# Kernel optimization log

Measured on AMD Instinct MI355X. Metric: run time of the kernel, lower is better.

The kernel has to match this reference:

```python
import jax, jax.numpy as jnp
import numpy as np

GROUPS = 32
N_HEADS = 16
EPS = 1e-5


def setup_inputs() -> dict:
    key = jax.random.key(0)
    ks = jax.random.split(key, 5)
    b, c, t = 4, 1024, 1024
    return {
        "x": jax.random.normal(ks[0], (b, c, t), dtype=jnp.float32),
        "gn_weight": jnp.ones((c,), dtype=jnp.float32),
        "gn_bias": jnp.zeros((c,), dtype=jnp.float32),
        "qkv_w": jax.random.normal(ks[1], (3 * c, c), dtype=jnp.float32) * (c ** -0.5),
        "qkv_b": jax.random.normal(ks[2], (3 * c,), dtype=jnp.float32) * 0.02,
        "proj_w": jax.random.normal(ks[3], (c, c), dtype=jnp.float32) * (c ** -0.5),
        "proj_b": jax.random.normal(ks[4], (c,), dtype=jnp.float32) * 0.02,
    }


def _group_norm(x, weight, bias):
    # x: [b, c, t]; GroupNorm32 computes stats in float32 (already fp32 here)
    b, c, t = x.shape
    xg = x.reshape(b, GROUPS, c // GROUPS, t)
    mean = xg.mean(axis=(2, 3), keepdims=True)
    var = xg.var(axis=(2, 3), keepdims=True)
    xn = ((xg - mean) * jax.lax.rsqrt(var + EPS)).reshape(b, c, t)
    return xn * weight[None, :, None] + bias[None, :, None]


def reference(x, gn_weight, gn_bias, qkv_w, qkv_b, proj_w, proj_b):
    b, c, t = x.shape
    xn = _group_norm(x, gn_weight, gn_bias)
    # 1x1 Conv1d == channel matmul: [3c, c] x [b, c, t] -> [b, 3c, t]
    qkv = jnp.einsum('oc,bct->bot', qkv_w, xn) + qkv_b[None, :, None]
    ch = c // N_HEADS
    # legacy per-head interleaved layout: reshape to [b*H, 3*ch, t], split
    qkv = qkv.reshape(b * N_HEADS, 3 * ch, t)
    q, k, v = qkv[:, :ch], qkv[:, ch:2 * ch], qkv[:, 2 * ch:]
    scale = ch ** -0.25  # 1/sqrt(sqrt(ch)), applied to both q and k
    weight = jnp.einsum('bct,bcs->bts', q * scale, k * scale)  # [b*H, t, t]
    weight = jax.nn.softmax(weight.astype(jnp.float32), axis=-1).astype(weight.dtype)
    a = jnp.einsum('bts,bcs->bct', weight, v).reshape(b, c, t)
    h = jnp.einsum('oc,bct->bot', proj_w, a) + proj_b[None, :, None]
    return x + h
```

## Files before the change

### kernel.cpp

```cpp
#include <hip/hip_runtime.h>
#include <hip/hip_bf16.h>

typedef __bf16 bf16;
typedef __bf16 bf16x2 __attribute__((ext_vector_type(2)));
typedef __bf16 bf16x4 __attribute__((ext_vector_type(4)));
typedef __bf16 bf16x8 __attribute__((ext_vector_type(8)));
typedef float  f32x4  __attribute__((ext_vector_type(4)));

static __device__ __forceinline__ f32x4 mfma16(bf16x8 a, bf16x8 b, f32x4 c) {
  return __builtin_amdgcn_mfma_f32_16x16x32_bf16(a, b, c, 0, 0, 0);
}

static __device__ __forceinline__ void gload_lds16(const bf16* g, bf16* l) {
  __builtin_amdgcn_global_load_lds(
      (const __attribute__((address_space(1))) void*)g,
      (__attribute__((address_space(3))) void*)l, 16, 0, 0);
}

#define VMCNT0() asm volatile("s_waitcnt vmcnt(0)" ::: "memory")
#define BARRIER()                                        \
  do {                                                   \
    __builtin_amdgcn_sched_barrier(0);                   \
    asm volatile("" ::: "memory");                       \
    __builtin_amdgcn_s_barrier();                        \
    asm volatile("" ::: "memory");                       \
    __builtin_amdgcn_sched_barrier(0);                   \
  } while (0)

__global__ __launch_bounds__(256) void cvt2_kernel(const float* __restrict__ wa,
                                                   bf16* __restrict__ oa,
                                                   const float* __restrict__ wb,
                                                   bf16* __restrict__ ob) {
  int i = blockIdx.x * 256 + threadIdx.x;
  const int na4 = 3072 * 1024 / 4;
  const float* src; bf16* dst;
  if (i < na4) { src = wa; dst = oa; }
  else         { src = wb; dst = ob; i -= na4; }
  float4 v = ((const float4*)src)[i];
  bf16x4 o = { (bf16)v.x, (bf16)v.y, (bf16)v.z, (bf16)v.w };
  *(bf16x4*)(dst + 4ll * i) = o;
}

__global__ __launch_bounds__(512) void gn_kernel(const float* __restrict__ x,
                                                 const float* __restrict__ w,
                                                 const float* __restrict__ bias,
                                                 bf16* __restrict__ xnT) {
  int id = blockIdx.x;
  int b = id >> 7, g = (id >> 2) & 31, qtr = id & 3;
  const float* xb = x + ((size_t)b * 1024 + g * 32) * 1024;
  int tid = threadIdx.x;
  float s = 0.f, sq = 0.f;
  const float4* x4 = (const float4*)xb;
  for (int i = tid; i < 8192; i += 512) {
    float4 v = x4[i];
    s  += v.x + v.y + v.z + v.w;
    sq += v.x * v.x + v.y * v.y + v.z * v.z + v.w * v.w;
  }
#pragma unroll
  for (int off = 32; off; off >>= 1) { s += __shfl_down(s, off); sq += __shfl_down(sq, off); }
  __shared__ float red[16];
  int wv = tid >> 6;
  if ((tid & 63) == 0) { red[wv] = s; red[8 + wv] = sq; }
  __syncthreads();
  s = 0.f; sq = 0.f;
#pragma unroll
  for (int i = 0; i < 8; ++i) { s += red[i]; sq += red[8 + i]; }
  float mean = s * (1.f / 32768.f);
  float var  = sq * (1.f / 32768.f) - mean * mean;
  float rstd = rsqrtf(var + 1e-5f);

  __shared__ bf16 tile[64][36];
  int c = tid >> 4, q = tid & 15;
  int r = tid >> 3, q2 = tid & 7;
  float wc = w[g * 32 + c] * rstd;
  float fb = bias[g * 32 + c] - mean * wc;
  for (int t0 = qtr * 256; t0 < qtr * 256 + 256; t0 += 64) {
    float4 v = *(const float4*)(xb + (size_t)c * 1024 + t0 + q * 4);
    tile[q * 4 + 0][c] = (bf16)(v.x * wc + fb);
    tile[q * 4 + 1][c] = (bf16)(v.y * wc + fb);
    tile[q * 4 + 2][c] = (bf16)(v.z * wc + fb);
    tile[q * 4 + 3][c] = (bf16)(v.w * wc + fb);
    __syncthreads();
    *(bf16x4*)&xnT[((size_t)b * 1024 + t0 + r) * 1024 + g * 32 + q2 * 4] =
        *(bf16x4*)&tile[r][q2 * 4];
    __syncthreads();
  }
}

__global__ __launch_bounds__(512, 1) void qkv_kernel(
    const bf16* __restrict__ A, const bf16* __restrict__ Bw,
    const float* __restrict__ bias,
    bf16* __restrict__ qkT, bf16* __restrict__ vC) {
  extern __shared__ __align__(16) bf16 smem[];

  int tid = threadIdx.x, wid = tid >> 6, lane = tid & 63;
  int l15 = lane & 15, l4 = lane >> 4;
  int wr = wid >> 2, wc = wid & 3;
  int rsw = (l15 & 7) << 4;

  int sid = (blockIdx.x & 7) * 32 + (blockIdx.x >> 3);
  int bx = sid & 15, by = (sid >> 4) & 3, z = sid >> 6;
  int m0 = by * 256, n0 = bx * 192;
  const bf16* Ab = A + (size_t)z * 1024 * 1024 + (size_t)m0 * 1024;
  const bf16* Bb = Bw + (size_t)n0 * 1024;

  int srow = tid >> 3;
  int csw  = (tid & 7) ^ (srow & 7);
  auto stageA = [&](int d, int h, int kt) {
    bf16* dst = smem + d * 16384 + h * 8192;
    const bf16* src = Ab + (size_t)(h * 128) * 1024 + kt * 64 + csw * 8;
#pragma unroll
    for (int L = 0; L < 2; ++L)
      gload_lds16(src + (size_t)(L * 64 + srow) * 1024, dst + (L * 512 + wid * 64) * 8);
  };
  auto stageB = [&](int d, int kt) {
    bf16* dst = smem + 32768 + d * 12288;
    const bf16* src = Bb + kt * 64 + csw * 8;
#pragma unroll
    for (int L = 0; L < 3; ++L)
      gload_lds16(src + (size_t)(L * 64 + srow) * 1024, dst + (L * 512 + wid * 64) * 8);
  };

  f32x4 acc[8][3] = {};

  stageA(0, 0, 0); stageA(0, 1, 0); stageB(0, 0);
  VMCNT0();
  BARRIER();

  for (int t = 0; t < 16; ++t) {
    int d = t & 1;
    const char* Ab8 = (const char*)smem + d * 32768 + wr * 16384;
    const char* Bb8 = (const char*)smem + 65536 + d * 24576;

    bf16x8 bfr[3][2], af[4][2];
#pragma unroll
    for (int ni = 0; ni < 3; ++ni) {
      int rb = (wc * 48 + ni * 16 + l15) * 128;
#pragma unroll
      for (int kk = 0; kk < 2; ++kk)
        bfr[ni][kk] = *(const bf16x8*)(Bb8 + rb + ((kk * 64 + l4 * 16) ^ rsw));
    }
#pragma unroll
    for (int mi = 0; mi < 4; ++mi) {
      int rb = (mi * 16 + l15) * 128;
#pragma unroll
      for (int kk = 0; kk < 2; ++kk)
        af[mi][kk] = *(const bf16x8*)(Ab8 + rb + ((kk * 64 + l4 * 16) ^ rsw));
    }
    if (t < 15) { stageA(d ^ 1, 0, t + 1); stageA(d ^ 1, 1, t + 1); }
    BARRIER();
    __builtin_amdgcn_s_setprio(1);
#pragma unroll
    for (int mi = 0; mi < 4; ++mi)
#pragma unroll
      for (int ni = 0; ni < 3; ++ni)
#pragma unroll
        for (int kk = 0; kk < 2; ++kk)
          acc[mi][ni] = mfma16(af[mi][kk], bfr[ni][kk], acc[mi][ni]);
    __builtin_amdgcn_s_setprio(0);
    BARRIER();

#pragma unroll
    for (int mi = 0; mi < 4; ++mi) {
      int rb = ((4 + mi) * 16 + l15) * 128;
#pragma unroll
      for (int kk = 0; kk < 2; ++kk)
        af[mi][kk] = *(const bf16x8*)(Ab8 + rb + ((kk * 64 + l4 * 16) ^ rsw));
    }
    if (t < 15) stageB(d ^ 1, t + 1);
    BARRIER();
    __builtin_amdgcn_s_setprio(1);
#pragma unroll
    for (int mi = 0; mi < 4; ++mi)
#pragma unroll
      for (int ni = 0; ni < 3; ++ni)
#pragma unroll
        for (int kk = 0; kk < 2; ++kk)
          acc[4 + mi][ni] = mfma16(af[mi][kk], bfr[ni][kk], acc[4 + mi][ni]);
    __builtin_amdgcn_s_setprio(0);
    VMCNT0();
    BARRIER();
  }

  const float scale = 0.35355339059327373f;
  int h = bx;
#pragma unroll
  for (int ni = 0; ni < 3; ++ni) {
    int oin = wc * 48 + ni * 16;
    float bv = bias[n0 + oin + l15];
#pragma unroll
    for (int mi = 0; mi < 8; ++mi) {
      int tb = m0 + wr * 128 + mi * 16 + l4 * 4;
      f32x4 v = acc[mi][ni];
      if (oin < 128) {
#pragma unroll
        for (int i = 0; i < 4; ++i)
          qkT[((size_t)z * 1024 + tb + i) * 2048 + h * 128 + oin + l15] =
              (bf16)((v[i] + bv) * scale);
      } else {
        bf16x4 st = { (bf16)(v[0] + bv), (bf16)(v[1] + bv),
                      (bf16)(v[2] + bv), (bf16)(v[3] + bv) };
        *(bf16x4*)&vC[(((size_t)z * 16 + h) * 64 + (oin - 128 + l15)) * 1024 + tb] = st;
      }
    }
  }
}

template <int MODE>
__global__ __launch_bounds__(256) void gemm_kernel(
    const bf16* __restrict__ A, const bf16* __restrict__ Bw,
    const float* __restrict__ bias,
    bf16* __restrict__ qkT, bf16* __restrict__ vC,
    const float* __restrict__ xres, float* __restrict__ out) {
  __shared__ bf16 At[128 * 32];
  __shared__ bf16 Bt[128 * 32];
  int tid = threadIdx.x;
  int wid = tid >> 6, lane = tid & 63;
  int l15 = lane & 15, l4 = lane >> 4;
  int wm = wid >> 1, wn = wid & 1;
  int z = blockIdx.z;
  int m0 = blockIdx.y * 128, n0 = blockIdx.x * 128;
  const bf16* Ab = A + (size_t)z * 1024 * 1024 + (size_t)m0 * 1024;
  const bf16* Bb = Bw + (size_t)n0 * 1024;

  f32x4 acc[4][4] = {};

  for (int k0 = 0; k0 < 1024; k0 += 32) {
#pragma unroll
    for (int j = 0; j < 2; ++j) {
      int slot = j * 256 + tid;
      int row  = slot >> 2;
      int ck   = (slot & 3) ^ ((row >> 1) & 3);
      gload_lds16(Ab + (size_t)row * 1024 + k0 + ck * 8, At + (size_t)(j * 256 + wid * 64) * 8);
      gload_lds16(Bb + (size_t)row * 1024 + k0 + ck * 8, Bt + (size_t)(j * 256 + wid * 64) * 8);
    }
    __syncthreads();
    bf16x8 af[4], bfr[4];
#pragma unroll
    for (int mi = 0; mi < 4; ++mi) {
      int row = wm * 64 + mi * 16 + l15;
      int ck  = l4 ^ ((row >> 1) & 3);
      af[mi] = *(const bf16x8*)(At + row * 32 + ck * 8);
    }
#pragma unroll
    for (int nf = 0; nf < 4; ++nf) {
      int row = wn * 64 + nf * 16 + l15;
      int ck  = l4 ^ ((row >> 1) & 3);
      bfr[nf] = *(const bf16x8*)(Bt + row * 32 + ck * 8);
    }
#pragma unroll
    for (int mi = 0; mi < 4; ++mi)
#pragma unroll
      for (int nf = 0; nf < 4; ++nf)
        acc[mi][nf] = mfma16(af[mi], bfr[nf], acc[mi][nf]);
    __syncthreads();
  }

  if (MODE == 1) {
#pragma unroll
    for (int nf = 0; nf < 4; ++nf) {
      int o = n0 + wn * 64 + nf * 16 + l15;
      float bv = bias[o];
#pragma unroll
      for (int mi = 0; mi < 4; ++mi) {
        int tb = m0 + wm * 64 + mi * 16 + l4 * 4;
        size_t base = ((size_t)z * 1024 + o) * 1024 + tb;
        float4 xr = *(const float4*)(xres + base);
        f32x4 v = acc[mi][nf];
        float4 ov = { xr.x + v[0] + bv, xr.y + v[1] + bv,
                      xr.z + v[2] + bv, xr.w + v[3] + bv };
        *(float4*)(out + base) = ov;
      }
    }
  }
}

__global__ __launch_bounds__(512, 4) void attn_kernel(const bf16* __restrict__ qkT,
                                                      const bf16* __restrict__ vC,
                                                      bf16* __restrict__ aT) {
  __shared__ __align__(16) bf16 Kt[2][64 * 64];
  __shared__ __align__(16) bf16 Vt[2][64 * 64];
  __shared__ __align__(16) bf16 Pt[8][16 * 64];

  int id = blockIdx.x;
  int sid = (id & 7) * 64 + (id >> 3);
  int head = sid >> 3, tblk = sid & 7;
  int b = head >> 4, h = head & 15;
  int t0 = tblk * 128;
  int tid = threadIdx.x, wid = tid >> 6, lane = tid & 63;
  int l15 = lane & 15, l4 = lane >> 4;
  int trow = t0 + wid * 16;

  const bf16* kbase = qkT + (size_t)b * 1024 * 2048 + h * 128 + 64;
  const bf16* vbase = vC + (size_t)(b * 16 + h) * 64 * 1024;
  char* Pw = (char*)Pt[wid];
  int rsw = (l15 & 7) << 4;
  char* PwRow = Pw + l15 * 128;

  const bf16* qrow = qkT + ((size_t)b * 1024 + trow + l15) * 2048 + h * 128;
  bf16x8 qf[2];
#pragma unroll
  for (int kb = 0; kb < 2; ++kb) qf[kb] = *(const bf16x8*)(qrow + kb * 32 + l4 * 8);

  int rl = lane >> 3;
  int scol = (((lane & 7) * 16) ^ (rl << 4)) >> 1;
  int r8 = wid * 8 + rl;
  auto stage = [&](int buf, int st) {
    int s0 = st * 64;
    gload_lds16(kbase + (size_t)(s0 + r8) * 2048 + scol, &Kt[buf][wid * 512]);
    gload_lds16(vbase + (size_t)r8 * 1024 + s0 + scol, &Vt[buf][wid * 512]);
  };

  float m_run = -1e30f, l_run = 0.f;
  f32x4 oacc[4] = {};

  stage(0, 0);
  __syncthreads();

  for (int st = 0; st < 16; ++st) {
    int cur = st & 1;
    if (st < 15) stage(cur ^ 1, st + 1);

    const char* Kb = (const char*)Kt[cur];
    f32x4 sf[4];
#pragma unroll
    for (int nf = 0; nf < 4; ++nf) sf[nf] = (f32x4){0.f, 0.f, 0.f, 0.f};
    __builtin_amdgcn_s_setprio(1);
#pragma unroll
    for (int nf = 0; nf < 4; ++nf) {
      int rr = nf * 16 + l15;
#pragma unroll
      for (int kb = 0; kb < 2; ++kb) {
        bf16x8 kf = *(const bf16x8*)(Kb + rr * 128 + ((kb * 64 + l4 * 16) ^ rsw));
        sf[nf] = mfma16(kf, qf[kb], sf[nf]);
      }
    }
    __builtin_amdgcn_s_setprio(0);

    float mb;
    {
      float a0 = fmaxf(fmaxf(sf[0][0], sf[0][1]), fmaxf(sf[0][2], sf[0][3]));
      float a1 = fmaxf(fmaxf(sf[1][0], sf[1][1]), fmaxf(sf[1][2], sf[1][3]));
      float a2 = fmaxf(fmaxf(sf[2][0], sf[2][1]), fmaxf(sf[2][2], sf[2][3]));
      float a3 = fmaxf(fmaxf(sf[3][0], sf[3][1]), fmaxf(sf[3][2], sf[3][3]));
      mb = fmaxf(fmaxf(a0, a1), fmaxf(a2, a3));
    }
    mb = fmaxf(mb, __shfl_xor(mb, 16));
    mb = fmaxf(mb, __shfl_xor(mb, 32));
    if (!__all(mb - m_run <= 8.f)) {
      float mn = fmaxf(m_run, mb);
      float corr = __expf(m_run - mn);
      m_run = mn;
      l_run *= corr;
#pragma unroll
      for (int cf = 0; cf < 4; ++cf)
#pragma unroll
        for (int i = 0; i < 4; ++i) oacc[cf][i] *= corr;
    }
    float sb = 0.f;
#pragma unroll
    for (int nf = 0; nf < 4; ++nf) {
      float p0 = __expf(sf[nf][0] - m_run), p1 = __expf(sf[nf][1] - m_run);
      float p2 = __expf(sf[nf][2] - m_run), p3 = __expf(sf[nf][3] - m_run);
      sb += (p0 + p1) + (p2 + p3);
      int off = nf * 32 + l4 * 8;
      *(bf16x4*)(PwRow + (off ^ rsw)) = (bf16x4){ (bf16)p0, (bf16)p1, (bf16)p2, (bf16)p3 };
    }
    sb += __shfl_xor(sb, 16);
    sb += __shfl_xor(sb, 32);
    l_run += sb;

    const char* Vb = (const char*)Vt[cur];
    __builtin_amdgcn_s_setprio(1);
#pragma unroll
    for (int kb = 0; kb < 2; ++kb) {
      bf16x8 pf = *(const bf16x8*)(Pw + l15 * 128 + ((kb * 64 + l4 * 16) ^ rsw));
#pragma unroll
      for (int cf = 0; cf < 4; ++cf) {
        int rr = cf * 16 + l15;
        bf16x8 vf = *(const bf16x8*)(Vb + rr * 128 + ((kb * 64 + l4 * 16) ^ rsw));
        oacc[cf] = mfma16(vf, pf, oacc[cf]);
      }
    }
    __builtin_amdgcn_s_setprio(0);
    __syncthreads();
  }

  float rdiv = 1.f / l_run;
  int t = trow + l15;
#pragma unroll
  for (int cf = 0; cf < 4; ++cf) {
    bf16x4 ov = { (bf16)(oacc[cf][0] * rdiv), (bf16)(oacc[cf][1] * rdiv),
                  (bf16)(oacc[cf][2] * rdiv), (bf16)(oacc[cf][3] * rdiv) };
    *(bf16x4*)&aT[((size_t)b * 1024 + t) * 1024 + h * 64 + cf * 16 + l4 * 4] = ov;
  }
}

extern "C" void kernel_launch(void* const* d_in, const int* in_sizes, int n_in,
                              void* d_out, int out_size, void* d_ws, size_t ws_size,
                              hipStream_t stream) {
  const float* x      = (const float*)d_in[0];
  const float* gw     = (const float*)d_in[1];
  const float* gb     = (const float*)d_in[2];
  const float* qkv_w  = (const float*)d_in[3];
  const float* qkv_b  = (const float*)d_in[4];
  const float* proj_w = (const float*)d_in[5];
  const float* proj_b = (const float*)d_in[6];
  float* out = (float*)d_out;

  char* ws = (char*)d_ws;
  bf16* wq_bf = (bf16*)(ws);
  bf16* wp_bf = (bf16*)(ws + 6ll  * 1024 * 1024);
  bf16* xnT   = (bf16*)(ws + 8ll  * 1024 * 1024);
  bf16* qkT   = (bf16*)(ws + 16ll * 1024 * 1024);
  bf16* vC    = (bf16*)(ws + 32ll * 1024 * 1024);
  bf16* aT    = (bf16*)(ws + 40ll * 1024 * 1024);

  hipFuncSetAttribute(reinterpret_cast<const void*>(qkv_kernel),
                      hipFuncAttributeMaxDynamicSharedMemorySize, 114688);

  cvt2_kernel<<<dim3(4096), dim3(256), 0, stream>>>(qkv_w, wq_bf, proj_w, wp_bf);
  gn_kernel<<<dim3(512), dim3(512), 0, stream>>>(x, gw, gb, xnT);
  qkv_kernel<<<dim3(256), dim3(512), 114688, stream>>>(xnT, wq_bf, qkv_b, qkT, vC);
  attn_kernel<<<dim3(512), dim3(512), 0, stream>>>(qkT, vC, aT);
  gemm_kernel<1><<<dim3(8, 8, 4), dim3(256), 0, stream>>>(aT, wp_bf, proj_b, nullptr, nullptr, x, out);
}
```

Measured before the change: 108.7 us.

## Process 32 query rows per wave in attention to reuse K/V fragments

The attention kernel now uses 4 waves per block instead of 8, and each wave handles two 16-row query groups. Each K and V fragment read from LDS feeds two MFMAs, which halves LDS read traffic per unit of compute. Each thread also issues twice as many staging loads. The cost is higher register pressure (doubled accumulators and score tiles) and fewer waves per block to hide latency; launch bounds change to 256 threads with a minimum of 2 blocks per SM.

```diff
diff --git a/kernel.cpp b/kernel.cpp
--- a/kernel.cpp
+++ b/kernel.cpp
@@ -275,12 +275,12 @@
   }
 }
 
-__global__ __launch_bounds__(512, 4) void attn_kernel(const bf16* __restrict__ qkT,
+__global__ __launch_bounds__(256, 2) void attn_kernel(const bf16* __restrict__ qkT,
                                                       const bf16* __restrict__ vC,
                                                       bf16* __restrict__ aT) {
   __shared__ __align__(16) bf16 Kt[2][64 * 64];
   __shared__ __align__(16) bf16 Vt[2][64 * 64];
-  __shared__ __align__(16) bf16 Pt[8][16 * 64];
+  __shared__ __align__(16) bf16 Pt[4][32 * 64];
 
   int id = blockIdx.x;
   int sid = (id & 7) * 64 + (id >> 3);
@@ -289,30 +289,36 @@
   int t0 = tblk * 128;
   int tid = threadIdx.x, wid = tid >> 6, lane = tid & 63;
   int l15 = lane & 15, l4 = lane >> 4;
-  int trow = t0 + wid * 16;
+  int trow = t0 + wid * 32;
 
   const bf16* kbase = qkT + (size_t)b * 1024 * 2048 + h * 128 + 64;
   const bf16* vbase = vC + (size_t)(b * 16 + h) * 64 * 1024;
   char* Pw = (char*)Pt[wid];
   int rsw = (l15 & 7) << 4;
-  char* PwRow = Pw + l15 * 128;
-
-  const bf16* qrow = qkT + ((size_t)b * 1024 + trow + l15) * 2048 + h * 128;
-  bf16x8 qf[2];
-#pragma unroll
-  for (int kb = 0; kb < 2; ++kb) qf[kb] = *(const bf16x8*)(qrow + kb * 32 + l4 * 8);
+
+  bf16x8 qf[2][2];
+#pragma unroll
+  for (int g = 0; g < 2; ++g) {
+    const bf16* qrow = qkT + ((size_t)b * 1024 + trow + g * 16 + l15) * 2048 + h * 128;
+#pragma unroll
+    for (int kb = 0; kb < 2; ++kb) qf[g][kb] = *(const bf16x8*)(qrow + kb * 32 + l4 * 8);
+  }
 
   int rl = lane >> 3;
   int scol = (((lane & 7) * 16) ^ (rl << 4)) >> 1;
-  int r8 = wid * 8 + rl;
   auto stage = [&](int buf, int st) {
     int s0 = st * 64;
-    gload_lds16(kbase + (size_t)(s0 + r8) * 2048 + scol, &Kt[buf][wid * 512]);
-    gload_lds16(vbase + (size_t)r8 * 1024 + s0 + scol, &Vt[buf][wid * 512]);
+#pragma unroll
+    for (int j = 0; j < 2; ++j) {
+      int g8 = wid * 2 + j;
+      int r = g8 * 8 + rl;
+      gload_lds16(kbase + (size_t)(s0 + r) * 2048 + scol, &Kt[buf][g8 * 512]);
+      gload_lds16(vbase + (size_t)r * 1024 + s0 + scol, &Vt[buf][g8 * 512]);
+    }
   };
 
-  float m_run = -1e30f, l_run = 0.f;
-  f32x4 oacc[4] = {};
+  float m_run[2] = { -1e30f, -1e30f }, l_run[2] = { 0.f, 0.f };
+  f32x4 oacc[4][2] = {};
 
   stage(0, 0);
   __syncthreads();
@@ -322,9 +328,11 @@
     if (st < 15) stage(cur ^ 1, st + 1);
 
     const char* Kb = (const char*)Kt[cur];
-    f32x4 sf[4];
-#pragma unroll
-    for (int nf = 0; nf < 4; ++nf) sf[nf] = (f32x4){0.f, 0.f, 0.f, 0.f};
+    f32x4 sf[4][2];
+#pragma unroll
+    for (int nf = 0; nf < 4; ++nf)
+#pragma unroll
+      for (int g = 0; g < 2; ++g) sf[nf][g] = (f32x4){0.f, 0.f, 0.f, 0.f};
     __builtin_amdgcn_s_setprio(1);
 #pragma unroll
     for (int nf = 0; nf < 4; ++nf) {
@@ -332,67 +340,82 @@
 #pragma unroll
       for (int kb = 0; kb < 2; ++kb) {
         bf16x8 kf = *(const bf16x8*)(Kb + rr * 128 + ((kb * 64 + l4 * 16) ^ rsw));
-        sf[nf] = mfma16(kf, qf[kb], sf[nf]);
+        sf[nf][0] = mfma16(kf, qf[0][kb], sf[nf][0]);
+        sf[nf][1] = mfma16(kf, qf[1][kb], sf[nf][1]);
       }
     }
     __builtin_amdgcn_s_setprio(0);
 
-    float mb;
-    {
-      float a0 = fmaxf(fmaxf(sf[0][0], sf[0][1]), fmaxf(sf[0][2], sf[0][3]));
-      float a1 = fmaxf(fmaxf(sf[1][0], sf[1][1]), fmaxf(sf[1][2], sf[1][3]));
-      float a2 = fmaxf(fmaxf(sf[2][0], sf[2][1]), fmaxf(sf[2][2], sf[2][3]));
-      float a3 = fmaxf(fmaxf(sf[3][0], sf[3][1]), fmaxf(sf[3][2], sf[3][3]));
-      mb = fmaxf(fmaxf(a0, a1), fmaxf(a2, a3));
-    }
-    mb = fmaxf(mb, __shfl_xor(mb, 16));
-    mb = fmaxf(mb, __shfl_xor(mb, 32));
-    if (!__all(mb - m_run <= 8.f)) {
-      float mn = fmaxf(m_run, mb);
-      float corr = __expf(m_run - mn);
-      m_run = mn;
-      l_run *= corr;
-#pragma unroll
-      for (int cf = 0; cf < 4; ++cf)
-#pragma unroll
-        for (int i = 0; i < 4; ++i) oacc[cf][i] *= corr;
-    }
-    float sb = 0.f;
-#pragma unroll
-    for (int nf = 0; nf < 4; ++nf) {
-      float p0 = __expf(sf[nf][0] - m_run), p1 = __expf(sf[nf][1] - m_run);
-      float p2 = __expf(sf[nf][2] - m_run), p3 = __expf(sf[nf][3] - m_run);
-      sb += (p0 + p1) + (p2 + p3);
-      int off = nf * 32 + l4 * 8;
-      *(bf16x4*)(PwRow + (off ^ rsw)) = (bf16x4){ (bf16)p0, (bf16)p1, (bf16)p2, (bf16)p3 };
-    }
-    sb += __shfl_xor(sb, 16);
-    sb += __shfl_xor(sb, 32);
-    l_run += sb;
+    float mb[2];
+#pragma unroll
+    for (int g = 0; g < 2; ++g) {
+      float a0 = fmaxf(fmaxf(sf[0][g][0], sf[0][g][1]), fmaxf(sf[0][g][2], sf[0][g][3]));
+      float a1 = fmaxf(fmaxf(sf[1][g][0], sf[1][g][1]), fmaxf(sf[1][g][2], sf[1][g][3]));
+      float a2 = fmaxf(fmaxf(sf[2][g][0], sf[2][g][1]), fmaxf(sf[2][g][2], sf[2][g][3]));
+      float a3 = fmaxf(fmaxf(sf[3][g][0], sf[3][g][1]), fmaxf(sf[3][g][2], sf[3][g][3]));
+      float m = fmaxf(fmaxf(a0, a1), fmaxf(a2, a3));
+      m = fmaxf(m, __shfl_xor(m, 16));
+      mb[g] = fmaxf(m, __shfl_xor(m, 32));
+    }
+    float dmax = fmaxf(mb[0] - m_run[0], mb[1] - m_run[1]);
+    if (!__all(dmax <= 8.f)) {
+#pragma unroll
+      for (int g = 0; g < 2; ++g) {
+        float mn = fmaxf(m_run[g], mb[g]);
+        float corr = __expf(m_run[g] - mn);
+        m_run[g] = mn;
+        l_run[g] *= corr;
+#pragma unroll
+        for (int cf = 0; cf < 4; ++cf)
+#pragma unroll
+          for (int i = 0; i < 4; ++i) oacc[cf][g][i] *= corr;
+      }
+    }
+#pragma unroll
+    for (int g = 0; g < 2; ++g) {
+      char* PwRow = Pw + (g * 16 + l15) * 128;
+      float sb = 0.f;
+#pragma unroll
+      for (int nf = 0; nf < 4; ++nf) {
+        float p0 = __expf(sf[nf][g][0] - m_run[g]), p1 = __expf(sf[nf][g][1] - m_run[g]);
+        float p2 = __expf(sf[nf][g][2] - m_run[g]), p3 = __expf(sf[nf][g][3] - m_run[g]);
+        sb += (p0 + p1) + (p2 + p3);
+        int off = nf * 32 + l4 * 8;
+        *(bf16x4*)(PwRow + (off ^ rsw)) = (bf16x4){ (bf16)p0, (bf16)p1, (bf16)p2, (bf16)p3 };
+      }
+      sb += __shfl_xor(sb, 16);
+      sb += __shfl_xor(sb, 32);
+      l_run[g] += sb;
+    }
 
     const char* Vb = (const char*)Vt[cur];
     __builtin_amdgcn_s_setprio(1);
 #pragma unroll
     for (int kb = 0; kb < 2; ++kb) {
-      bf16x8 pf = *(const bf16x8*)(Pw + l15 * 128 + ((kb * 64 + l4 * 16) ^ rsw));
+      bf16x8 pf0 = *(const bf16x8*)(Pw + l15 * 128 + ((kb * 64 + l4 * 16) ^ rsw));
+      bf16x8 pf1 = *(const bf16x8*)(Pw + (16 + l15) * 128 + ((kb * 64 + l4 * 16) ^ rsw));
 #pragma unroll
       for (int cf = 0; cf < 4; ++cf) {
         int rr = cf * 16 + l15;
         bf16x8 vf = *(const bf16x8*)(Vb + rr * 128 + ((kb * 64 + l4 * 16) ^ rsw));
-        oacc[cf] = mfma16(vf, pf, oacc[cf]);
+        oacc[cf][0] = mfma16(vf, pf0, oacc[cf][0]);
+        oacc[cf][1] = mfma16(vf, pf1, oacc[cf][1]);
       }
     }
     __builtin_amdgcn_s_setprio(0);
     __syncthreads();
   }
 
-  float rdiv = 1.f / l_run;
-  int t = trow + l15;
-#pragma unroll
-  for (int cf = 0; cf < 4; ++cf) {
-    bf16x4 ov = { (bf16)(oacc[cf][0] * rdiv), (bf16)(oacc[cf][1] * rdiv),
-                  (bf16)(oacc[cf][2] * rdiv), (bf16)(oacc[cf][3] * rdiv) };
-    *(bf16x4*)&aT[((size_t)b * 1024 + t) * 1024 + h * 64 + cf * 16 + l4 * 4] = ov;
+#pragma unroll
+  for (int g = 0; g < 2; ++g) {
+    float rdiv = 1.f / l_run[g];
+    int t = trow + g * 16 + l15;
+#pragma unroll
+    for (int cf = 0; cf < 4; ++cf) {
+      bf16x4 ov = { (bf16)(oacc[cf][g][0] * rdiv), (bf16)(oacc[cf][g][1] * rdiv),
+                    (bf16)(oacc[cf][g][2] * rdiv), (bf16)(oacc[cf][g][3] * rdiv) };
+      *(bf16x4*)&aT[((size_t)b * 1024 + t) * 1024 + h * 64 + cf * 16 + l4 * 4] = ov;
+    }
   }
 }
 
@@ -422,6 +445,6 @@
   cvt2_kernel<<<dim3(4096), dim3(256), 0, stream>>>(qkv_w, wq_bf, proj_w, wp_bf);
   gn_kernel<<<dim3(512), dim3(512), 0, stream>>>(x, gw, gb, xnT);
   qkv_kernel<<<dim3(256), dim3(512), 114688, stream>>>(xnT, wq_bf, qkv_b, qkT, vC);
-  attn_kernel<<<dim3(512), dim3(512), 0, stream>>>(qkT, vC, aT);
+  attn_kernel<<<dim3(512), dim3(256), 0, stream>>>(qkT, vC, aT);
   gemm_kernel<1><<<dim3(8, 8, 4), dim3(256), 0, stream>>>(aT, wp_bf, proj_b, nullptr, nullptr, x, out);
 }
```

Result: no change. 110.6 us (+1.8%).
